# Performance work log

Measured on AMD Instinct MI355X. Metric: run time of the kernel, lower is better.

## Reference

```python
import jax, jax.numpy as jnp
import numpy as np

N = 100000   # nodes
E = 1600000  # edges
D = 128      # hidden dim
L = 3        # message-passing layers
OUT = 128


def setup_inputs() -> dict:
    key = jax.random.key(0)
    ks = jax.random.split(key, 6)
    x = jax.random.normal(ks[0], (N, D), dtype=jnp.float32)
    edge_index = jax.random.randint(ks[1], (2, E), 0, N, dtype=jnp.int64)
    s = 1.0 / np.sqrt(D)
    conv_w = jax.random.normal(ks[2], (L, D, D), dtype=jnp.float32) * s
    conv_b = jax.random.normal(ks[3], (L, D), dtype=jnp.float32) * 0.01
    lin_w = jax.random.normal(ks[4], (OUT, D * (L + 1)), dtype=jnp.float32) * (1.0 / np.sqrt(D * (L + 1)))
    lin_b = jax.random.normal(ks[5], (OUT,), dtype=jnp.float32) * 0.01
    return {"x": x, "edge_index": edge_index, "conv_w": conv_w,
            "conv_b": conv_b, "lin_w": lin_w, "lin_b": lin_b}


def reference(x, edge_index, conv_w, conv_b, lin_w, lin_b):
    n = x.shape[0]
    # PyG GCNConv: add self-loops, symmetric normalization deg^{-1/2}
    loop = jnp.arange(n, dtype=edge_index.dtype)
    src = jnp.concatenate([edge_index[0], loop])  # [E+N] message sources
    dst = jnp.concatenate([edge_index[1], loop])  # [E+N] message targets
    deg = jax.ops.segment_sum(jnp.ones_like(src, dtype=x.dtype), dst, num_segments=n)
    dinv = jnp.where(deg > 0, jax.lax.rsqrt(deg), 0.0)
    norm = (dinv[src] * dinv[dst])[:, None]  # [E+N, 1]

    def gcn_conv(h, W, b):
        hw = h @ W.T                      # [N, D] linear (bias=False)
        msg = hw[src] * norm              # gather + edge-normalize
        agg = jax.ops.segment_sum(msg, dst, num_segments=n)  # scatter-add
        return agg + b

    h_list = [x]
    for l in range(conv_w.shape[0]):
        h = jax.nn.elu(gcn_conv(h_list[l], conv_w[l], conv_b[l]))
        h = h + h_list[l]                 # residual
        h_list.append(h)
    node_repr = jnp.concatenate(h_list, axis=1)  # [N, D*(L+1)]
    return node_repr @ lin_w.T + lin_b
```

## Files before the change

### kernel.cpp

```cpp
#include <hip/hip_runtime.h>
#include <hip/hip_bf16.h>
#include <math.h>

typedef __bf16 bf16x8 __attribute__((ext_vector_type(8)));
typedef float f32x4 __attribute__((ext_vector_type(4)));
typedef unsigned int uint32;
typedef unsigned short ushort16;

#define TILE1 2048

__device__ inline float bfl(uint32 v) { return __uint_as_float(v << 16); }
__device__ inline float bfh(uint32 v) { return __uint_as_float(v & 0xffff0000u); }
__device__ inline ushort16 f2bf(float f) {
  __bf16 b = (__bf16)f;
  return __builtin_bit_cast(ushort16, b);
}
__device__ inline float bf2f(ushort16 u) { return __uint_as_float(((uint32)u) << 16); }


__global__ __launch_bounds__(256) void hist1_kernel(const int* __restrict__ ei, int E,
                                                    int nT1, int nb1, int* __restrict__ histT) {
  __shared__ int h[512];
  int t = threadIdx.x;
  for (int b = t; b < 512; b += 256) h[b] = 0;
  __syncthreads();
  int base = blockIdx.x * TILE1;
  int end = min(base + TILE1, E);
  for (int e = base + t; e < end; e += 256) {
    int d = ei[E + e];
    atomicAdd(&h[d >> 9], 1);
  }
  __syncthreads();
  for (int b = t; b < nb1; b += 256) histT[b * nT1 + blockIdx.x] = h[b];
}

__global__ __launch_bounds__(256) void scan1_kernel(const int* __restrict__ in,
                                                    int* __restrict__ out,
                                                    int* __restrict__ bsums, int m) {
  __shared__ int sdata[256];
  int t = threadIdx.x;
  int base = blockIdx.x * 1024;
  int v[4]; int s = 0;
#pragma unroll
  for (int c = 0; c < 4; ++c) {
    int idx = base + t * 4 + c;
    v[c] = (idx < m) ? in[idx] : 0;
    s += v[c];
  }
  sdata[t] = s;
  __syncthreads();
  for (int off = 1; off < 256; off <<= 1) {
    int y = (t >= off) ? sdata[t - off] : 0;
    __syncthreads();
    sdata[t] += y;
    __syncthreads();
  }
  int run = sdata[t] - s;
#pragma unroll
  for (int c = 0; c < 4; ++c) {
    int idx = base + t * 4 + c;
    if (idx < m) out[idx] = run;
    run += v[c];
  }
  if (t == 255) bsums[blockIdx.x] = sdata[255];
}

__global__ __launch_bounds__(256) void scan2_kernel(int* bsums, int nb) {
  __shared__ int sd[256];
  int t = threadIdx.x;
  int v = (t < nb) ? bsums[t] : 0;
  sd[t] = v;
  __syncthreads();
  for (int off = 1; off < 256; off <<= 1) {
    int y = (t >= off) ? sd[t - off] : 0;
    __syncthreads();
    sd[t] += y;
    __syncthreads();
  }
  if (t < nb) bsums[t] = sd[t] - v;
}

__global__ void scan_add_kernel(int* __restrict__ out, const int* __restrict__ bsums, int m) {
  int stride = gridDim.x * blockDim.x;
  for (int i = blockIdx.x * blockDim.x + threadIdx.x; i < m; i += stride)
    out[i] += bsums[i >> 10];
}

__global__ __launch_bounds__(256) void scatter1_kernel(const int* __restrict__ ei, int E,
                                                       int nT1, int nb1,
                                                       const int* __restrict__ histS,
                                                       uint32* __restrict__ pkT) {
  __shared__ int base[512];
  int t = threadIdx.x;
  for (int b = t; b < nb1; b += 256) base[b] = histS[b * nT1 + blockIdx.x];
  __syncthreads();
  int s0 = blockIdx.x * TILE1;
  int end = min(s0 + TILE1, E);
  for (int e = s0 + t; e < end; e += 256) {
    int d = ei[E + e];
    int s = ei[e];
    int p = atomicAdd(&base[d >> 9], 1);
    pkT[p] = ((uint32)(d & 511) << 20) | (uint32)s;
  }
}

__global__ __launch_bounds__(256) void pass2_kernel(
    const uint32* __restrict__ pkT, const int* __restrict__ histS, int nT1, int nb1,
    int E, int n, int* __restrict__ col_src, int* __restrict__ row_ptr,
    float* __restrict__ dinv) {
  __shared__ int hist[512];
  __shared__ int offs[512];
  __shared__ int sdata[256];
  int b = blockIdx.x;
  int t = threadIdx.x;
  int bstart = histS[b * nT1];
  int bend = (b + 1 < nb1) ? histS[(b + 1) * nT1] : E;
  for (int i = t; i < 512; i += 256) hist[i] = 0;
  __syncthreads();
  for (int e = bstart + t; e < bend; e += 256)
    atomicAdd(&hist[pkT[e] >> 20], 1);
  __syncthreads();
  int s2 = hist[2 * t] + hist[2 * t + 1];
  sdata[t] = s2;
  __syncthreads();
  for (int off = 1; off < 256; off <<= 1) {
    int y = (t >= off) ? sdata[t - off] : 0;
    __syncthreads();
    sdata[t] += y;
    __syncthreads();
  }
  int excl = sdata[t] - s2;
  offs[2 * t] = excl;
  offs[2 * t + 1] = excl + hist[2 * t];
  __syncthreads();
  for (int i = t; i < 512; i += 256) {
    int node = (b << 9) + i;
    if (node < n) {
      row_ptr[node] = bstart + offs[i];
      dinv[node] = rsqrtf((float)hist[i] + 1.0f);
    }
  }
  __syncthreads();
  for (int e = bstart + t; e < bend; e += 256) {
    uint32 pk = pkT[e];
    int p = atomicAdd(&offs[pk >> 20], 1);
    col_src[bstart + p] = (int)(pk & 0xFFFFFu);
  }
}

__global__ void finalize_rowptr_kernel(int* row_ptr, int n, int E) {
  if (threadIdx.x == 0 && blockIdx.x == 0) row_ptr[n] = E;
}


__global__ void cast_w_kernel(const float* __restrict__ cw, int total,
                              __bf16* __restrict__ whi) {
  int stride = gridDim.x * blockDim.x;
  for (int i = blockIdx.x * blockDim.x + threadIdx.x; i < total; i += stride)
    whi[i] = (__bf16)cw[i];
}

__global__ void cumw_kernel(const float* __restrict__ lw, __bf16* __restrict__ CB,
                            int parts) {
  int idx = blockIdx.x * blockDim.x + threadIdx.x;
  if (idx >= parts * 16384) return;
  int p = idx >> 14, o = (idx >> 7) & 127, k = idx & 127;
  float s = 0.f;
  for (int l = p; l < parts; ++l) s += lw[o * (parts * 128) + l * 128 + k];
  CB[idx] = (__bf16)s;
}

__global__ void init_h_kernel(const float* __restrict__ x, __bf16* __restrict__ h_hi,
                              __bf16* __restrict__ h_lo, long total) {
  long stride = (long)gridDim.x * blockDim.x;
  for (long i = blockIdx.x * (long)blockDim.x + threadIdx.x; i < total; i += stride) {
    float v = x[i];
    __bf16 hi = (__bf16)v;
    h_hi[i] = hi;
    h_lo[i] = (__bf16)(v - (float)hi);
  }
}

__global__ __launch_bounds__(512) void gemm_conv_kernel(
    const __bf16* __restrict__ a_hi, const __bf16* __restrict__ a_lo,
    const __bf16* __restrict__ w1, const float* __restrict__ row_scale,
    ushort16* __restrict__ C1, int n) {
  __shared__ __bf16 smem[16384];
  int t = threadIdx.x;
  int wv = t >> 6;
  int l = t & 63;
  int r = l & 15;
  int g = l >> 4;
  int row0 = blockIdx.x * 128 + wv * 16;
  int arow = row0 + r;
  if (arow >= n) arow = n - 1;

  bf16x8 ah[4], al[4];
#pragma unroll
  for (int kc = 0; kc < 4; ++kc) {
    ah[kc] = *(const bf16x8*)(a_hi + (long)arow * 128 + kc * 32 + g * 8);
    al[kc] = *(const bf16x8*)(a_lo + (long)arow * 128 + kc * 32 + g * 8);
  }
#pragma unroll
  for (int i = 0; i < 4; ++i) {
    int G = i * 512 + t;
    int col = G >> 4, ch = G & 15;
    bf16x8 v = *(const bf16x8*)(w1 + (long)col * 128 + ch * 8);
    *(bf16x8*)(smem + col * 128 + ((ch ^ (col & 7)) << 3)) = v;
  }
  __syncthreads();

  f32x4 acc[8];
#pragma unroll
  for (int i = 0; i < 8; ++i) acc[i] = (f32x4){0.f, 0.f, 0.f, 0.f};
#pragma unroll
  for (int kc = 0; kc < 4; ++kc) {
#pragma unroll
    for (int nt = 0; nt < 8; ++nt) {
      int col = nt * 16 + r;
      bf16x8 f1 = *(const bf16x8*)(smem + col * 128 + (((kc * 4 + g) ^ (col & 7)) << 3));
      acc[nt] = __builtin_amdgcn_mfma_f32_16x16x32_bf16(ah[kc], f1, acc[nt], 0, 0, 0);
      acc[nt] = __builtin_amdgcn_mfma_f32_16x16x32_bf16(al[kc], f1, acc[nt], 0, 0, 0);
    }
  }

  int orow0 = row0 + g * 4;
  float rs[4];
#pragma unroll
  for (int q = 0; q < 4; ++q) {
    int gr = orow0 + q;
    rs[q] = (gr < n) ? row_scale[gr] : 0.f;
  }
#pragma unroll
  for (int nt = 0; nt < 8; ++nt) {
    int col = nt * 16 + r;
#pragma unroll
    for (int q = 0; q < 4; ++q) {
      int gr = orow0 + q;
      if (gr < n) C1[(long)gr * 128 + col] = f2bf(acc[nt][q] * rs[q]);
    }
  }
}

__global__ __launch_bounds__(512) void gemm_final_kernel(
    const float* __restrict__ x, const __bf16* __restrict__ eA,
    const __bf16* __restrict__ eB, const __bf16* __restrict__ eC,
    const __bf16* __restrict__ CB, float* __restrict__ out,
    const float* __restrict__ bias, int n) {
  __shared__ __bf16 smem[16384];
  int t = threadIdx.x;
  int wv = t >> 6;
  int l = t & 63;
  int r = l & 15;
  int g = l >> 4;
  int row0 = blockIdx.x * 128 + wv * 16;
  int arow = row0 + r;
  if (arow >= n) arow = n - 1;

  f32x4 acc[8];
#pragma unroll
  for (int i = 0; i < 8; ++i) acc[i] = (f32x4){0.f, 0.f, 0.f, 0.f};

  for (int p = 0; p < 4; ++p) {
    __syncthreads();
#pragma unroll
    for (int i = 0; i < 4; ++i) {
      int G = i * 512 + t;
      int col = G >> 4, ch = G & 15;
      bf16x8 v = *(const bf16x8*)(CB + p * 16384 + col * 128 + ch * 8);
      *(bf16x8*)(smem + col * 128 + ((ch ^ (col & 7)) << 3)) = v;
    }
    __syncthreads();

    bf16x8 af[4];
    if (p == 0) {
#pragma unroll
      for (int kc = 0; kc < 4; ++kc) {
        float4 f0 = *(const float4*)(x + (long)arow * 128 + kc * 32 + g * 8);
        float4 f1 = *(const float4*)(x + (long)arow * 128 + kc * 32 + g * 8 + 4);
        bf16x8 v;
        v[0] = (__bf16)f0.x; v[1] = (__bf16)f0.y; v[2] = (__bf16)f0.z; v[3] = (__bf16)f0.w;
        v[4] = (__bf16)f1.x; v[5] = (__bf16)f1.y; v[6] = (__bf16)f1.z; v[7] = (__bf16)f1.w;
        af[kc] = v;
      }
    } else {
      const __bf16* ep = (p == 1) ? eA : (p == 2) ? eB : eC;
#pragma unroll
      for (int kc = 0; kc < 4; ++kc)
        af[kc] = *(const bf16x8*)(ep + (long)arow * 128 + kc * 32 + g * 8);
    }
#pragma unroll
    for (int kc = 0; kc < 4; ++kc) {
#pragma unroll
      for (int nt = 0; nt < 8; ++nt) {
        int col = nt * 16 + r;
        bf16x8 f1 = *(const bf16x8*)(smem + col * 128 + (((kc * 4 + g) ^ (col & 7)) << 3));
        acc[nt] = __builtin_amdgcn_mfma_f32_16x16x32_bf16(af[kc], f1, acc[nt], 0, 0, 0);
      }
    }
  }

  int orow0 = row0 + g * 4;
#pragma unroll
  for (int nt = 0; nt < 8; ++nt) {
    int col = nt * 16 + r;
    float bv = bias[col];
#pragma unroll
    for (int q = 0; q < 4; ++q) {
      int gr = orow0 + q;
      if (gr < n) out[(long)gr * 128 + col] = acc[nt][q] + bv;
    }
  }
}

__global__ __launch_bounds__(256) void aggregate_kernel(
    const uint2* __restrict__ hw4, const int* __restrict__ col_src,
    const int* __restrict__ row_ptr, const float* __restrict__ dinv,
    const float* __restrict__ bias, uint2* __restrict__ h_hi4,
    uint2* __restrict__ h_lo4, uint2* __restrict__ e4, int n) {
  int wid = (blockIdx.x << 2) + (threadIdx.x >> 6);
  if (wid >= n) return;
  int lane = threadIdx.x & 63;
  int half = lane >> 5;
  int q = lane & 31;
  long rbase = (long)wid * 32;

  uint2 selfv = hw4[rbase + q];

  float a0 = 0.f, a1 = 0.f, a2 = 0.f, a3 = 0.f;
  int eb = row_ptr[wid], ee = row_ptr[wid + 1];
  int e = eb;
  for (; e + 8 <= ee; e += 8) {
    int s0 = col_src[e + 0 + half];
    int s1 = col_src[e + 2 + half];
    int s2 = col_src[e + 4 + half];
    int s3 = col_src[e + 6 + half];
    uint2 v0 = hw4[(long)s0 * 32 + q];
    uint2 v1 = hw4[(long)s1 * 32 + q];
    uint2 v2 = hw4[(long)s2 * 32 + q];
    uint2 v3 = hw4[(long)s3 * 32 + q];
    a0 += (bfl(v0.x) + bfl(v1.x)) + (bfl(v2.x) + bfl(v3.x));
    a1 += (bfh(v0.x) + bfh(v1.x)) + (bfh(v2.x) + bfh(v3.x));
    a2 += (bfl(v0.y) + bfl(v1.y)) + (bfl(v2.y) + bfl(v3.y));
    a3 += (bfh(v0.y) + bfh(v1.y)) + (bfh(v2.y) + bfh(v3.y));
  }
  for (; e < ee; e += 2) {
    int idx = e + half;
    if (idx < ee) {
      int s = col_src[idx];
      uint2 v = hw4[(long)s * 32 + q];
      a0 += bfl(v.x); a1 += bfh(v.x); a2 += bfl(v.y); a3 += bfh(v.y);
    }
  }
  a0 += __shfl_down(a0, 32, 64);
  a1 += __shfl_down(a1, 32, 64);
  a2 += __shfl_down(a2, 32, 64);
  a3 += __shfl_down(a3, 32, 64);
  if (half == 0) {
    a0 += bfl(selfv.x); a1 += bfh(selfv.x); a2 += bfl(selfv.y); a3 += bfh(selfv.y);
    float dv = dinv[wid];
    float4 bv = ((const float4*)bias)[q];
    float x0 = fmaf(a0, dv, bv.x);
    float x1 = fmaf(a1, dv, bv.y);
    float x2 = fmaf(a2, dv, bv.z);
    float x3 = fmaf(a3, dv, bv.w);
    float u0 = (x0 > 0.f) ? x0 : expm1f(x0);
    float u1 = (x1 > 0.f) ? x1 : expm1f(x1);
    float u2 = (x2 > 0.f) ? x2 : expm1f(x2);
    float u3 = (x3 > 0.f) ? x3 : expm1f(x3);
    uint2 ev;
    ev.x = (uint32)f2bf(u0) | ((uint32)f2bf(u1) << 16);
    ev.y = (uint32)f2bf(u2) | ((uint32)f2bf(u3) << 16);
    e4[rbase + q] = ev;
    uint2 hh = h_hi4[rbase + q];
    uint2 hl = h_lo4[rbase + q];
    float hv0 = bfl(hh.x) + bfl(hl.x) + u0;
    float hv1 = bfh(hh.x) + bfh(hl.x) + u1;
    float hv2 = bfl(hh.y) + bfl(hl.y) + u2;
    float hv3 = bfh(hh.y) + bfh(hl.y) + u3;
    ushort16 n0 = f2bf(hv0), n1 = f2bf(hv1), n2 = f2bf(hv2), n3 = f2bf(hv3);
    uint2 nh;
    nh.x = (uint32)n0 | ((uint32)n1 << 16);
    nh.y = (uint32)n2 | ((uint32)n3 << 16);
    h_hi4[rbase + q] = nh;
    float r0 = hv0 - bf2f(n0), r1 = hv1 - bf2f(n1);
    float r2 = hv2 - bf2f(n2), r3 = hv3 - bf2f(n3);
    uint2 nl;
    nl.x = (uint32)f2bf(r0) | ((uint32)f2bf(r1) << 16);
    nl.y = (uint32)f2bf(r2) | ((uint32)f2bf(r3) << 16);
    h_lo4[rbase + q] = nl;
  }
}


extern "C" void kernel_launch(void* const* d_in, const int* in_sizes, int n_in,
                              void* d_out, int out_size, void* d_ws, size_t ws_size,
                              hipStream_t stream) {
  const float* x      = (const float*)d_in[0];
  const int*   ei     = (const int*)d_in[1];
  const float* conv_w = (const float*)d_in[2];
  const float* conv_b = (const float*)d_in[3];
  const float* lin_w  = (const float*)d_in[4];
  const float* lin_b  = (const float*)d_in[5];
  float* out = (float*)d_out;

  const int n = in_sizes[0] / 128;
  const int E = in_sizes[1] / 2;
  const int L = in_sizes[2] / (128 * 128);
  const int cn = L * 128 * 128;

  const int nT1 = (E + TILE1 - 1) / TILE1;
  const int nb1 = (n + 511) >> 9;
  const int M = nb1 * nT1;
  const int nbs = (M + 1023) / 1024;

  char* p = (char*)d_ws;
  auto carve = [&](size_t bytes) {
    char* r = p;
    p += (bytes + 255) & ~(size_t)255;
    return r;
  };
  int*      histT   = (int*)carve((size_t)M * 4);
  int*      histS   = (int*)carve((size_t)M * 4);
  int*      bsums   = (int*)carve((size_t)nbs * 4);
  uint32*   pkT     = (uint32*)carve((size_t)E * 4);
  int*      col_src = (int*)carve((size_t)E * 4);
  int*      row_ptr = (int*)carve((size_t)(n + 1) * 4);
  float*    dinv    = (float*)carve((size_t)n * 4);
  ushort16* hw      = (ushort16*)carve((size_t)n * 128 * 2);
  __bf16*   h_hi    = (__bf16*)carve((size_t)n * 128 * 2);
  __bf16*   h_lo    = (__bf16*)carve((size_t)n * 128 * 2);
  __bf16*   e_all   = (__bf16*)carve((size_t)L * n * 128 * 2);
  __bf16*   w_conv  = (__bf16*)carve((size_t)cn * 2);
  __bf16*   CB      = (__bf16*)carve((size_t)(L + 1) * 16384 * 2);

  hist1_kernel<<<nT1, 256, 0, stream>>>(ei, E, nT1, nb1, histT);
  scan1_kernel<<<nbs, 256, 0, stream>>>(histT, histS, bsums, M);
  scan2_kernel<<<1, 256, 0, stream>>>(bsums, nbs);
  scan_add_kernel<<<(M + 65535) / 65536 * 256, 256, 0, stream>>>(histS, bsums, M);
  scatter1_kernel<<<nT1, 256, 0, stream>>>(ei, E, nT1, nb1, histS, pkT);
  pass2_kernel<<<nb1, 256, 0, stream>>>(pkT, histS, nT1, nb1, E, n,
                                        col_src, row_ptr, dinv);
  finalize_rowptr_kernel<<<1, 1, 0, stream>>>(row_ptr, n, E);

  cast_w_kernel<<<(cn + 255) / 256, 256, 0, stream>>>(conv_w, cn, w_conv);
  cumw_kernel<<<((L + 1) * 16384 + 255) / 256, 256, 0, stream>>>(lin_w, CB, L + 1);
  init_h_kernel<<<2048, 256, 0, stream>>>(x, h_hi, h_lo, (long)n * 128);

  int gblocks = (n + 127) / 128;
  for (int l = 0; l < L; ++l) {
    gemm_conv_kernel<<<gblocks, 512, 0, stream>>>(
        h_hi, h_lo, w_conv + (size_t)l * 128 * 128, dinv, hw, n);
    aggregate_kernel<<<(n + 3) / 4, 256, 0, stream>>>(
        (const uint2*)hw, col_src, row_ptr, dinv, conv_b + (size_t)l * 128,
        (uint2*)h_hi, (uint2*)h_lo, (uint2*)(e_all + (size_t)l * n * 128), n);
  }
  gemm_final_kernel<<<gblocks, 512, 0, stream>>>(
      x, e_all, e_all + (size_t)n * 128, e_all + (size_t)2 * n * 128,
      CB, out, lin_b, n);
}
```

Before: 533.7 us.

## Store residual state as fp32 and sort CSR columns by source sub-bucket

The residual hidden state is now kept as a single fp32 buffer instead of separate bf16 hi/lo buffers. The hi/lo split moves into the GEMM load path, which removes the init_h kernel and simplifies the aggregate epilogue to one float4 read-add-write. pass2 now bins edges by destination and by the high bits of the source, using a larger skewed shared-memory histogram, so each row's column list is roughly ordered by source. That ordering should improve gather locality in aggregation. In exchange, pass2 does more shared-memory work and a serial 32-entry scan per thread, and the GEMM converts fp32 to hi/lo on every load.

```diff
diff --git a/kernel.cpp b/kernel.cpp
--- a/kernel.cpp
+++ b/kernel.cpp
@@ -8,6 +8,7 @@
 typedef unsigned short ushort16;
 
 #define TILE1 2048
+#define TILES 16
 
 __device__ inline float bfl(uint32 v) { return __uint_as_float(v << 16); }
 __device__ inline float bfh(uint32 v) { return __uint_as_float(v & 0xffff0000u); }
@@ -15,7 +16,19 @@
   __bf16 b = (__bf16)f;
   return __builtin_bit_cast(ushort16, b);
 }
-__device__ inline float bf2f(ushort16 u) { return __uint_as_float(((uint32)u) << 16); }
+__device__ inline int sw(int b) { return (b & ~31) | ((b + (b >> 5)) & 31); }
+
+__device__ inline void split8(const float* __restrict__ p, bf16x8& hi, bf16x8& lo) {
+  float4 f0 = *(const float4*)p;
+  float4 f1 = *(const float4*)(p + 4);
+  float vv[8] = {f0.x, f0.y, f0.z, f0.w, f1.x, f1.y, f1.z, f1.w};
+#pragma unroll
+  for (int j = 0; j < 8; ++j) {
+    __bf16 h = (__bf16)vv[j];
+    hi[j] = h;
+    lo[j] = (__bf16)(vv[j] - (float)h);
+  }
+}
 
 
 __global__ __launch_bounds__(256) void hist1_kernel(const int* __restrict__ ei, int E,
@@ -108,20 +121,25 @@
     const uint32* __restrict__ pkT, const int* __restrict__ histS, int nT1, int nb1,
     int E, int n, int* __restrict__ col_src, int* __restrict__ row_ptr,
     float* __restrict__ dinv) {
-  __shared__ int hist[512];
-  __shared__ int offs[512];
+  __shared__ int offs[512 * TILES];
   __shared__ int sdata[256];
   int b = blockIdx.x;
   int t = threadIdx.x;
   int bstart = histS[b * nT1];
   int bend = (b + 1 < nb1) ? histS[(b + 1) * nT1] : E;
-  for (int i = t; i < 512; i += 256) hist[i] = 0;
-  __syncthreads();
-  for (int e = bstart + t; e < bend; e += 256)
-    atomicAdd(&hist[pkT[e] >> 20], 1);
-  __syncthreads();
-  int s2 = hist[2 * t] + hist[2 * t + 1];
-  sdata[t] = s2;
+  int total = bend - bstart;
+  for (int i = t; i < 512 * TILES; i += 256) offs[i] = 0;
+  __syncthreads();
+  for (int e = bstart + t; e < bend; e += 256) {
+    uint32 pk = pkT[e];
+    int bin = (int)((pk >> 20) << 4) | (int)((pk & 0xFFFFFu) >> 13);
+    atomicAdd(&offs[sw(bin)], 1);
+  }
+  __syncthreads();
+  int cbase = t * 32;
+  int s = 0;
+  for (int c = 0; c < 32; ++c) s += offs[sw(cbase + c)];
+  sdata[t] = s;
   __syncthreads();
   for (int off = 1; off < 256; off <<= 1) {
     int y = (t >= off) ? sdata[t - off] : 0;
@@ -129,22 +147,30 @@
     sdata[t] += y;
     __syncthreads();
   }
-  int excl = sdata[t] - s2;
-  offs[2 * t] = excl;
-  offs[2 * t + 1] = excl + hist[2 * t];
+  int run = sdata[t] - s;
+  for (int c = 0; c < 32; ++c) {
+    int idx = sw(cbase + c);
+    int v = offs[idx];
+    offs[idx] = run;
+    run += v;
+  }
   __syncthreads();
   for (int i = t; i < 512; i += 256) {
     int node = (b << 9) + i;
     if (node < n) {
-      row_ptr[node] = bstart + offs[i];
-      dinv[node] = rsqrtf((float)hist[i] + 1.0f);
+      int st = offs[sw(i << 4)];
+      int nx = (i < 511) ? offs[sw((i + 1) << 4)] : total;
+      row_ptr[node] = bstart + st;
+      dinv[node] = rsqrtf((float)(nx - st) + 1.0f);
     }
   }
   __syncthreads();
   for (int e = bstart + t; e < bend; e += 256) {
     uint32 pk = pkT[e];
-    int p = atomicAdd(&offs[pk >> 20], 1);
-    col_src[bstart + p] = (int)(pk & 0xFFFFFu);
+    int src = (int)(pk & 0xFFFFFu);
+    int bin = (int)((pk >> 20) << 4) | (src >> 13);
+    int p = atomicAdd(&offs[sw(bin)], 1);
+    col_src[bstart + p] = src;
   }
 }
 
@@ -170,21 +196,9 @@
   CB[idx] = (__bf16)s;
 }
 
-__global__ void init_h_kernel(const float* __restrict__ x, __bf16* __restrict__ h_hi,
-                              __bf16* __restrict__ h_lo, long total) {
-  long stride = (long)gridDim.x * blockDim.x;
-  for (long i = blockIdx.x * (long)blockDim.x + threadIdx.x; i < total; i += stride) {
-    float v = x[i];
-    __bf16 hi = (__bf16)v;
-    h_hi[i] = hi;
-    h_lo[i] = (__bf16)(v - (float)hi);
-  }
-}
-
 __global__ __launch_bounds__(512) void gemm_conv_kernel(
-    const __bf16* __restrict__ a_hi, const __bf16* __restrict__ a_lo,
-    const __bf16* __restrict__ w1, const float* __restrict__ row_scale,
-    ushort16* __restrict__ C1, int n) {
+    const float* __restrict__ A, const __bf16* __restrict__ w1,
+    const float* __restrict__ row_scale, ushort16* __restrict__ C1, int n) {
   __shared__ __bf16 smem[16384];
   int t = threadIdx.x;
   int wv = t >> 6;
@@ -197,10 +211,9 @@
 
   bf16x8 ah[4], al[4];
 #pragma unroll
-  for (int kc = 0; kc < 4; ++kc) {
-    ah[kc] = *(const bf16x8*)(a_hi + (long)arow * 128 + kc * 32 + g * 8);
-    al[kc] = *(const bf16x8*)(a_lo + (long)arow * 128 + kc * 32 + g * 8);
-  }
+  for (int kc = 0; kc < 4; ++kc)
+    split8(A + (long)arow * 128 + kc * 32 + g * 8, ah[kc], al[kc]);
+
 #pragma unroll
   for (int i = 0; i < 4; ++i) {
     int G = i * 512 + t;
@@ -276,12 +289,9 @@
     if (p == 0) {
 #pragma unroll
       for (int kc = 0; kc < 4; ++kc) {
-        float4 f0 = *(const float4*)(x + (long)arow * 128 + kc * 32 + g * 8);
-        float4 f1 = *(const float4*)(x + (long)arow * 128 + kc * 32 + g * 8 + 4);
-        bf16x8 v;
-        v[0] = (__bf16)f0.x; v[1] = (__bf16)f0.y; v[2] = (__bf16)f0.z; v[3] = (__bf16)f0.w;
-        v[4] = (__bf16)f1.x; v[5] = (__bf16)f1.y; v[6] = (__bf16)f1.z; v[7] = (__bf16)f1.w;
-        af[kc] = v;
+        bf16x8 hi, lo;
+        split8(x + (long)arow * 128 + kc * 32 + g * 8, hi, lo);
+        af[kc] = hi;
       }
     } else {
       const __bf16* ep = (p == 1) ? eA : (p == 2) ? eB : eC;
@@ -316,8 +326,8 @@
 __global__ __launch_bounds__(256) void aggregate_kernel(
     const uint2* __restrict__ hw4, const int* __restrict__ col_src,
     const int* __restrict__ row_ptr, const float* __restrict__ dinv,
-    const float* __restrict__ bias, uint2* __restrict__ h_hi4,
-    uint2* __restrict__ h_lo4, uint2* __restrict__ e4, int n) {
+    const float* __restrict__ bias, const float4* __restrict__ h_in,
+    float4* __restrict__ h_out, uint2* __restrict__ e4, int n) {
   int wid = (blockIdx.x << 2) + (threadIdx.x >> 6);
   if (wid >= n) return;
   int lane = threadIdx.x & 63;
@@ -372,23 +382,9 @@
     ev.x = (uint32)f2bf(u0) | ((uint32)f2bf(u1) << 16);
     ev.y = (uint32)f2bf(u2) | ((uint32)f2bf(u3) << 16);
     e4[rbase + q] = ev;
-    uint2 hh = h_hi4[rbase + q];
-    uint2 hl = h_lo4[rbase + q];
-    float hv0 = bfl(hh.x) + bfl(hl.x) + u0;
-    float hv1 = bfh(hh.x) + bfh(hl.x) + u1;
-    float hv2 = bfl(hh.y) + bfl(hl.y) + u2;
-    float hv3 = bfh(hh.y) + bfh(hl.y) + u3;
-    ushort16 n0 = f2bf(hv0), n1 = f2bf(hv1), n2 = f2bf(hv2), n3 = f2bf(hv3);
-    uint2 nh;
-    nh.x = (uint32)n0 | ((uint32)n1 << 16);
-    nh.y = (uint32)n2 | ((uint32)n3 << 16);
-    h_hi4[rbase + q] = nh;
-    float r0 = hv0 - bf2f(n0), r1 = hv1 - bf2f(n1);
-    float r2 = hv2 - bf2f(n2), r3 = hv3 - bf2f(n3);
-    uint2 nl;
-    nl.x = (uint32)f2bf(r0) | ((uint32)f2bf(r1) << 16);
-    nl.y = (uint32)f2bf(r2) | ((uint32)f2bf(r3) << 16);
-    h_lo4[rbase + q] = nl;
+    float4 hv = h_in[rbase + q];
+    hv.x += u0; hv.y += u1; hv.z += u2; hv.w += u3;
+    h_out[rbase + q] = hv;
   }
 }
 
@@ -428,8 +424,7 @@
   int*      row_ptr = (int*)carve((size_t)(n + 1) * 4);
   float*    dinv    = (float*)carve((size_t)n * 4);
   ushort16* hw      = (ushort16*)carve((size_t)n * 128 * 2);
-  __bf16*   h_hi    = (__bf16*)carve((size_t)n * 128 * 2);
-  __bf16*   h_lo    = (__bf16*)carve((size_t)n * 128 * 2);
+  float*    h       = (float*)carve((size_t)n * 128 * 4);
   __bf16*   e_all   = (__bf16*)carve((size_t)L * n * 128 * 2);
   __bf16*   w_conv  = (__bf16*)carve((size_t)cn * 2);
   __bf16*   CB      = (__bf16*)carve((size_t)(L + 1) * 16384 * 2);
@@ -445,15 +440,15 @@
 
   cast_w_kernel<<<(cn + 255) / 256, 256, 0, stream>>>(conv_w, cn, w_conv);
   cumw_kernel<<<((L + 1) * 16384 + 255) / 256, 256, 0, stream>>>(lin_w, CB, L + 1);
-  init_h_kernel<<<2048, 256, 0, stream>>>(x, h_hi, h_lo, (long)n * 128);
 
   int gblocks = (n + 127) / 128;
   for (int l = 0; l < L; ++l) {
+    const float* h_prev = (l == 0) ? x : h;
     gemm_conv_kernel<<<gblocks, 512, 0, stream>>>(
-        h_hi, h_lo, w_conv + (size_t)l * 128 * 128, dinv, hw, n);
+        h_prev, w_conv + (size_t)l * 128 * 128, dinv, hw, n);
     aggregate_kernel<<<(n + 3) / 4, 256, 0, stream>>>(
         (const uint2*)hw, col_src, row_ptr, dinv, conv_b + (size_t)l * 128,
-        (uint2*)h_hi, (uint2*)h_lo, (uint2*)(e_all + (size_t)l * n * 128), n);
+        (const float4*)h_prev, (float4*)h, (uint2*)(e_all + (size_t)l * n * 128), n);
   }
   gemm_final_kernel<<<gblocks, 512, 0, stream>>>(
       x, e_all, e_all + (size_t)n * 128, e_all + (size_t)2 * n * 128,
```

Result: faster. 516.8 us (-3.2%).

## Rebuild residual hidden state in GEMM from x plus stored ELU outputs

Applied to the files above, without the earlier changes.

Drops the separate hi/lo bf16 split of the hidden state and the init kernel. The conv GEMM now reconstructs h on the fly as x plus the previously stored bf16 ELU outputs, then splits it into hi/lo parts in registers. The aggregate kernel no longer reads and writes the h_hi and h_lo buffers, and it gains a 16-edge unrolled gather loop for more memory-level parallelism. The trade-off is extra reads of x and up to two e buffers inside the GEMM, plus small precision differences because the residual is summed from bf16 e values.

```diff
diff --git a/kernel.cpp b/kernel.cpp
--- a/kernel.cpp
+++ b/kernel.cpp
@@ -15,7 +15,6 @@
   __bf16 b = (__bf16)f;
   return __builtin_bit_cast(ushort16, b);
 }
-__device__ inline float bf2f(ushort16 u) { return __uint_as_float(((uint32)u) << 16); }
 
 
 __global__ __launch_bounds__(256) void hist1_kernel(const int* __restrict__ ei, int E,
@@ -170,21 +169,10 @@
   CB[idx] = (__bf16)s;
 }
 
-__global__ void init_h_kernel(const float* __restrict__ x, __bf16* __restrict__ h_hi,
-                              __bf16* __restrict__ h_lo, long total) {
-  long stride = (long)gridDim.x * blockDim.x;
-  for (long i = blockIdx.x * (long)blockDim.x + threadIdx.x; i < total; i += stride) {
-    float v = x[i];
-    __bf16 hi = (__bf16)v;
-    h_hi[i] = hi;
-    h_lo[i] = (__bf16)(v - (float)hi);
-  }
-}
-
 __global__ __launch_bounds__(512) void gemm_conv_kernel(
-    const __bf16* __restrict__ a_hi, const __bf16* __restrict__ a_lo,
-    const __bf16* __restrict__ w1, const float* __restrict__ row_scale,
-    ushort16* __restrict__ C1, int n) {
+    const float* __restrict__ X, const __bf16* __restrict__ E0,
+    const __bf16* __restrict__ E1, const __bf16* __restrict__ w1,
+    const float* __restrict__ row_scale, ushort16* __restrict__ C1, int n) {
   __shared__ __bf16 smem[16384];
   int t = threadIdx.x;
   int wv = t >> 6;
@@ -198,9 +186,28 @@
   bf16x8 ah[4], al[4];
 #pragma unroll
   for (int kc = 0; kc < 4; ++kc) {
-    ah[kc] = *(const bf16x8*)(a_hi + (long)arow * 128 + kc * 32 + g * 8);
-    al[kc] = *(const bf16x8*)(a_lo + (long)arow * 128 + kc * 32 + g * 8);
-  }
+    long off = (long)arow * 128 + kc * 32 + g * 8;
+    float4 f0 = *(const float4*)(X + off);
+    float4 f1 = *(const float4*)(X + off + 4);
+    float vv[8] = {f0.x, f0.y, f0.z, f0.w, f1.x, f1.y, f1.z, f1.w};
+    if (E0) {
+      bf16x8 tv = *(const bf16x8*)(E0 + off);
+#pragma unroll
+      for (int j = 0; j < 8; ++j) vv[j] += (float)tv[j];
+    }
+    if (E1) {
+      bf16x8 tv = *(const bf16x8*)(E1 + off);
+#pragma unroll
+      for (int j = 0; j < 8; ++j) vv[j] += (float)tv[j];
+    }
+#pragma unroll
+    for (int j = 0; j < 8; ++j) {
+      __bf16 hb = (__bf16)vv[j];
+      ah[kc][j] = hb;
+      al[kc][j] = (__bf16)(vv[j] - (float)hb);
+    }
+  }
+
 #pragma unroll
   for (int i = 0; i < 4; ++i) {
     int G = i * 512 + t;
@@ -276,8 +283,9 @@
     if (p == 0) {
 #pragma unroll
       for (int kc = 0; kc < 4; ++kc) {
-        float4 f0 = *(const float4*)(x + (long)arow * 128 + kc * 32 + g * 8);
-        float4 f1 = *(const float4*)(x + (long)arow * 128 + kc * 32 + g * 8 + 4);
+        long off = (long)arow * 128 + kc * 32 + g * 8;
+        float4 f0 = *(const float4*)(x + off);
+        float4 f1 = *(const float4*)(x + off + 4);
         bf16x8 v;
         v[0] = (__bf16)f0.x; v[1] = (__bf16)f0.y; v[2] = (__bf16)f0.z; v[3] = (__bf16)f0.w;
         v[4] = (__bf16)f1.x; v[5] = (__bf16)f1.y; v[6] = (__bf16)f1.z; v[7] = (__bf16)f1.w;
@@ -316,8 +324,7 @@
 __global__ __launch_bounds__(256) void aggregate_kernel(
     const uint2* __restrict__ hw4, const int* __restrict__ col_src,
     const int* __restrict__ row_ptr, const float* __restrict__ dinv,
-    const float* __restrict__ bias, uint2* __restrict__ h_hi4,
-    uint2* __restrict__ h_lo4, uint2* __restrict__ e4, int n) {
+    const float* __restrict__ bias, uint2* __restrict__ e4, int n) {
   int wid = (blockIdx.x << 2) + (threadIdx.x >> 6);
   if (wid >= n) return;
   int lane = threadIdx.x & 63;
@@ -330,15 +337,24 @@
   float a0 = 0.f, a1 = 0.f, a2 = 0.f, a3 = 0.f;
   int eb = row_ptr[wid], ee = row_ptr[wid + 1];
   int e = eb;
+  for (; e + 16 <= ee; e += 16) {
+    int s[8];
+#pragma unroll
+    for (int u = 0; u < 8; ++u) s[u] = col_src[e + 2 * u + half];
+    uint2 v[8];
+#pragma unroll
+    for (int u = 0; u < 8; ++u) v[u] = hw4[(long)s[u] * 32 + q];
+#pragma unroll
+    for (int u = 0; u < 8; ++u) {
+      a0 += bfl(v[u].x); a1 += bfh(v[u].x);
+      a2 += bfl(v[u].y); a3 += bfh(v[u].y);
+    }
+  }
   for (; e + 8 <= ee; e += 8) {
-    int s0 = col_src[e + 0 + half];
-    int s1 = col_src[e + 2 + half];
-    int s2 = col_src[e + 4 + half];
-    int s3 = col_src[e + 6 + half];
-    uint2 v0 = hw4[(long)s0 * 32 + q];
-    uint2 v1 = hw4[(long)s1 * 32 + q];
-    uint2 v2 = hw4[(long)s2 * 32 + q];
-    uint2 v3 = hw4[(long)s3 * 32 + q];
+    int s0 = col_src[e + 0 + half], s1 = col_src[e + 2 + half];
+    int s2 = col_src[e + 4 + half], s3 = col_src[e + 6 + half];
+    uint2 v0 = hw4[(long)s0 * 32 + q], v1 = hw4[(long)s1 * 32 + q];
+    uint2 v2 = hw4[(long)s2 * 32 + q], v3 = hw4[(long)s3 * 32 + q];
     a0 += (bfl(v0.x) + bfl(v1.x)) + (bfl(v2.x) + bfl(v3.x));
     a1 += (bfh(v0.x) + bfh(v1.x)) + (bfh(v2.x) + bfh(v3.x));
     a2 += (bfl(v0.y) + bfl(v1.y)) + (bfl(v2.y) + bfl(v3.y));
@@ -372,23 +388,6 @@
     ev.x = (uint32)f2bf(u0) | ((uint32)f2bf(u1) << 16);
     ev.y = (uint32)f2bf(u2) | ((uint32)f2bf(u3) << 16);
     e4[rbase + q] = ev;
-    uint2 hh = h_hi4[rbase + q];
-    uint2 hl = h_lo4[rbase + q];
-    float hv0 = bfl(hh.x) + bfl(hl.x) + u0;
-    float hv1 = bfh(hh.x) + bfh(hl.x) + u1;
-    float hv2 = bfl(hh.y) + bfl(hl.y) + u2;
-    float hv3 = bfh(hh.y) + bfh(hl.y) + u3;
-    ushort16 n0 = f2bf(hv0), n1 = f2bf(hv1), n2 = f2bf(hv2), n3 = f2bf(hv3);
-    uint2 nh;
-    nh.x = (uint32)n0 | ((uint32)n1 << 16);
-    nh.y = (uint32)n2 | ((uint32)n3 << 16);
-    h_hi4[rbase + q] = nh;
-    float r0 = hv0 - bf2f(n0), r1 = hv1 - bf2f(n1);
-    float r2 = hv2 - bf2f(n2), r3 = hv3 - bf2f(n3);
-    uint2 nl;
-    nl.x = (uint32)f2bf(r0) | ((uint32)f2bf(r1) << 16);
-    nl.y = (uint32)f2bf(r2) | ((uint32)f2bf(r3) << 16);
-    h_lo4[rbase + q] = nl;
   }
 }
 
@@ -428,11 +427,13 @@
   int*      row_ptr = (int*)carve((size_t)(n + 1) * 4);
   float*    dinv    = (float*)carve((size_t)n * 4);
   ushort16* hw      = (ushort16*)carve((size_t)n * 128 * 2);
-  __bf16*   h_hi    = (__bf16*)carve((size_t)n * 128 * 2);
-  __bf16*   h_lo    = (__bf16*)carve((size_t)n * 128 * 2);
   __bf16*   e_all   = (__bf16*)carve((size_t)L * n * 128 * 2);
   __bf16*   w_conv  = (__bf16*)carve((size_t)cn * 2);
   __bf16*   CB      = (__bf16*)carve((size_t)(L + 1) * 16384 * 2);
+
+  __bf16* e0 = e_all;
+  __bf16* e1 = e_all + (size_t)n * 128;
+  __bf16* e2 = e_all + (size_t)2 * n * 128;
 
   hist1_kernel<<<nT1, 256, 0, stream>>>(ei, E, nT1, nb1, histT);
   scan1_kernel<<<nbs, 256, 0, stream>>>(histT, histS, bsums, M);
@@ -445,17 +446,16 @@
 
   cast_w_kernel<<<(cn + 255) / 256, 256, 0, stream>>>(conv_w, cn, w_conv);
   cumw_kernel<<<((L + 1) * 16384 + 255) / 256, 256, 0, stream>>>(lin_w, CB, L + 1);
-  init_h_kernel<<<2048, 256, 0, stream>>>(x, h_hi, h_lo, (long)n * 128);
 
   int gblocks = (n + 127) / 128;
   for (int l = 0; l < L; ++l) {
     gemm_conv_kernel<<<gblocks, 512, 0, stream>>>(
-        h_hi, h_lo, w_conv + (size_t)l * 128 * 128, dinv, hw, n);
+        x, (l >= 1) ? e0 : nullptr, (l >= 2) ? e1 : nullptr,
+        w_conv + (size_t)l * 128 * 128, dinv, hw, n);
     aggregate_kernel<<<(n + 3) / 4, 256, 0, stream>>>(
         (const uint2*)hw, col_src, row_ptr, dinv, conv_b + (size_t)l * 128,
-        (uint2*)h_hi, (uint2*)h_lo, (uint2*)(e_all + (size_t)l * n * 128), n);
+        (uint2*)(e_all + (size_t)l * n * 128), n);
   }
   gemm_final_kernel<<<gblocks, 512, 0, stream>>>(
-      x, e_all, e_all + (size_t)n * 128, e_all + (size_t)2 * n * 128,
-      CB, out, lin_b, n);
-}
+      x, e0, e1, e2, CB, out, lin_b, n);
+}
```

Measured after the change: 498.2 us. -6.6%, faster.
